# Kernel tuning notes

Hardware: AMD Instinct MI355X
Metric: run time of the kernel (lower is better)

The kernel has to match this reference:

```python
import jax, jax.numpy as jnp
import numpy as np

B, S, H, OUT, STEPS = 64, 1024, 512, 256, 32


def setup_inputs() -> dict:
    key = jax.random.key(0)
    ks = jax.random.split(key, 10)
    s = 0.02
    return {
        "encoder_outputs": jax.random.normal(ks[0], (B, S, H), jnp.float32),
        "hidden": jax.random.normal(ks[1], (B, H), jnp.float32),
        # Attention: nn.Linear(2H, 1)
        "attn_w": jax.random.normal(ks[2], (2 * H,), jnp.float32) * s,
        "attn_b": jax.random.normal(ks[3], (1,), jnp.float32) * s,
        # LSTMCell(OUT + H, H): torch gate order i, f, g, o
        "w_ih": jax.random.normal(ks[4], (4 * H, OUT + H), jnp.float32) * s,
        "w_hh": jax.random.normal(ks[5], (4 * H, H), jnp.float32) * s,
        "b_ih": jax.random.normal(ks[6], (4 * H,), jnp.float32) * s,
        "b_hh": jax.random.normal(ks[7], (4 * H,), jnp.float32) * s,
        # fc: nn.Linear(H, OUT)
        "fc_w": jax.random.normal(ks[8], (OUT, H), jnp.float32) * s,
        "fc_b": jax.random.normal(ks[9], (OUT,), jnp.float32) * s,
    }


def reference(encoder_outputs, hidden, attn_w, attn_b, w_ih, w_hh, b_ih, b_hh, fc_w, fc_b):
    # Split attention weight: Linear(concat(enc, hid)) == enc@wa_e + hid@wa_d + b
    wa_e, wa_d = attn_w[:H], attn_w[H:]
    # encoder contribution to attention energy is step-invariant: [B, S]
    enc_energy = jnp.einsum("bsh,h->bs", encoder_outputs, wa_e) + attn_b[0]
    bias = b_ih + b_hh  # [4H]

    def step(carry, _):
        h, c, dec_in = carry
        # Bahdanau-style energy and context
        energy = enc_energy + (h @ wa_d)[:, None]          # [B, S]
        weights = jax.nn.softmax(energy, axis=1)
        context = jnp.einsum("bs,bsh->bh", weights, encoder_outputs)
        # LSTMCell (torch gate order i, f, g, o)
        x = jnp.concatenate([dec_in, context], axis=1)     # [B, OUT+H]
        gates = x @ w_ih.T + h @ w_hh.T + bias             # [B, 4H]
        i, f, g, o = jnp.split(gates, 4, axis=1)
        c_new = jax.nn.sigmoid(f) * c + jax.nn.sigmoid(i) * jnp.tanh(g)
        h_new = jax.nn.sigmoid(o) * jnp.tanh(c_new)
        dec_new = h_new @ fc_w.T + fc_b                    # [B, OUT]
        return (h_new, c_new, dec_new), dec_new

    dec0 = jnp.zeros((encoder_outputs.shape[0], fc_w.shape[0]), encoder_outputs.dtype)
    c0 = jnp.zeros_like(hidden)
    _, outs = jax.lax.scan(step, (hidden, c0, dec0), None, length=STEPS)
    return jnp.transpose(outs, (1, 0, 2))  # [B, STEPS, OUT]
```

## Files before the change

kernel.cpp:

```cpp
#include <hip/hip_runtime.h>
#include <math.h>

#define B 64
#define S 1024
#define H 512
#define OUT 256
#define STEPS 32
#define NG 2048
#define X 768

typedef __attribute__((ext_vector_type(8))) short short8;
typedef __attribute__((ext_vector_type(4))) short s16x4;
typedef __attribute__((ext_vector_type(4))) float f32x4;
typedef __attribute__((ext_vector_type(4))) unsigned u32x4;

__device__ __forceinline__ float sigf(float x) { return 1.0f / (1.0f + __expf(-x)); }
__device__ __forceinline__ float tanhf_fast(float x) {
  return 2.0f / (1.0f + __expf(-2.0f * x)) - 1.0f;
}

__device__ __forceinline__ short f2bf(float x) {
  union { float f; unsigned u; } a; a.f = x;
  unsigned r = a.u + 0x7fffu + ((a.u >> 16) & 1u);
  return (short)(r >> 16);
}
__device__ __forceinline__ float bf2f(short s) {
  union { unsigned u; float f; } a; a.u = ((unsigned)(unsigned short)s) << 16;
  return a.f;
}

__device__ __forceinline__ unsigned load_u32_cg(const unsigned* p) {
  unsigned r;
  asm volatile("global_load_dword %0, %1, off sc0 sc1\n\ts_waitcnt vmcnt(0)"
               : "=v"(r) : "v"(p) : "memory");
  return r;
}

__global__ __launch_bounds__(256) void k_pre(
    const float* __restrict__ enc, const float* __restrict__ attn_w,
    float* __restrict__ part_ctx, float* __restrict__ part_ml,
    const float* __restrict__ w_ih, const float* __restrict__ w_hh,
    const float* __restrict__ fc_w, short* __restrict__ whi,
    short* __restrict__ wlo) {
  __shared__ float smem[8320];
  const int cid = blockIdx.x;
  const int tid = threadIdx.x;
  if (cid < 512) {
    float* sm_acc = smem;
    float* sm_l = smem + 2048;
    const int b = cid >> 3, chunk = cid & 7;
    const int wave = tid >> 6, lane = tid & 63;
    const float4 wa0 = *(const float4*)(attn_w + lane * 8);
    const float4 wa1 = *(const float4*)(attn_w + lane * 8 + 4);
    const float* eb = enc + (long)b * S * H + (long)(chunk * 128 + wave) * H + lane * 8;
    float l = 0.0f;
    float acc[8];
#pragma unroll
    for (int r = 0; r < 8; ++r) acc[r] = 0.0f;
#pragma unroll 2
    for (int i = 0; i < 32; ++i) {
      const float* row = eb + (long)i * 4 * H;
      const float4 v0 = *(const float4*)row;
      const float4 v1 = *(const float4*)(row + 4);
      float e = v0.x * wa0.x + v0.y * wa0.y + v0.z * wa0.z + v0.w * wa0.w +
                v1.x * wa1.x + v1.y * wa1.y + v1.z * wa1.z + v1.w * wa1.w;
#pragma unroll
      for (int msk = 1; msk < 64; msk <<= 1) e += __shfl_xor(e, msk, 64);
      const float p = __expf(e);
      l += p;
      acc[0] = fmaf(p, v0.x, acc[0]); acc[1] = fmaf(p, v0.y, acc[1]);
      acc[2] = fmaf(p, v0.z, acc[2]); acc[3] = fmaf(p, v0.w, acc[3]);
      acc[4] = fmaf(p, v1.x, acc[4]); acc[5] = fmaf(p, v1.y, acc[5]);
      acc[6] = fmaf(p, v1.z, acc[6]); acc[7] = fmaf(p, v1.w, acc[7]);
    }
#pragma unroll
    for (int r = 0; r < 8; ++r) sm_acc[wave * 512 + lane * 8 + r] = acc[r];
    if (lane == 0) sm_l[wave] = l;
    __syncthreads();
    const int h0 = tid * 2;
    float s0 = 0.f, s1 = 0.f;
#pragma unroll
    for (int w = 0; w < 4; ++w) {
      s0 += sm_acc[w * 512 + h0];
      s1 += sm_acc[w * 512 + h0 + 1];
    }
    float* pc = part_ctx + ((long)chunk * B + b) * H;
    pc[h0] = s0; pc[h0 + 1] = s1;
    if (tid == 0)
      part_ml[chunk * B + b] = sm_l[0] + sm_l[1] + sm_l[2] + sm_l[3];
  } else {
    float* ft = smem;
    float* wd = smem + 4128;
    const int n0 = (cid - 512) * 16;
    for (int i = tid; i < 1024; i += 256) {
      const int r = i >> 6, c4 = (i & 63) << 2;
      *(float4*)&wd[r * 260 + c4] = *(const float4*)(w_ih + (long)(n0 + r) * X + c4);
    }
    float acc[2][16];
#pragma unroll
    for (int rg = 0; rg < 2; ++rg)
#pragma unroll
      for (int e = 0; e < 16; ++e) acc[rg][e] = 0.f;
    const int n_l = tid >> 5, kq = tid & 31;
    for (int jt = 0; jt < 32; ++jt) {
      __syncthreads();
      for (int i = tid; i < 1024; i += 256) {
        const int r = i >> 7, c4 = (i & 127) << 2;
        *(float4*)&ft[r * 516 + c4] =
            *(const float4*)(fc_w + (long)(jt * 8 + r) * H + c4);
      }
      __syncthreads();
#pragma unroll 2
      for (int j = 0; j < 8; ++j) {
        float4 f[4];
#pragma unroll
        for (int e4 = 0; e4 < 4; ++e4) f[e4] = *(float4*)&ft[j * 516 + kq * 4 + e4 * 128];
#pragma unroll
        for (int rg = 0; rg < 2; ++rg) {
          const float w = wd[(rg * 8 + n_l) * 260 + jt * 8 + j];
#pragma unroll
          for (int e4 = 0; e4 < 4; ++e4) {
            acc[rg][e4 * 4 + 0] = fmaf(w, f[e4].x, acc[rg][e4 * 4 + 0]);
            acc[rg][e4 * 4 + 1] = fmaf(w, f[e4].y, acc[rg][e4 * 4 + 1]);
            acc[rg][e4 * 4 + 2] = fmaf(w, f[e4].z, acc[rg][e4 * 4 + 2]);
            acc[rg][e4 * 4 + 3] = fmaf(w, f[e4].w, acc[rg][e4 * 4 + 3]);
          }
        }
      }
    }
#pragma unroll
    for (int rg = 0; rg < 2; ++rg) {
      const long rbase = (long)(n0 + rg * 8 + n_l) * H;
#pragma unroll
      for (int e4 = 0; e4 < 4; ++e4) {
        const int k = kq * 4 + e4 * 128;
        const float4 hh = *(const float4*)(w_hh + rbase + k);
        float v[4] = {acc[rg][e4 * 4] + hh.x, acc[rg][e4 * 4 + 1] + hh.y,
                      acc[rg][e4 * 4 + 2] + hh.z, acc[rg][e4 * 4 + 3] + hh.w};
        s16x4 hi4, lo4;
#pragma unroll
        for (int e = 0; e < 4; ++e) {
          const short hb = f2bf(v[e]);
          hi4[e] = hb;
          lo4[e] = f2bf(v[e] - bf2f(hb));
        }
        *(s16x4*)(whi + rbase + k) = hi4;
        *(s16x4*)(wlo + rbase + k) = lo4;
      }
    }
  }
}

__global__ __launch_bounds__(256) void k_gbase(
    const float* __restrict__ w_ih, const float* __restrict__ w_hh,
    const float* __restrict__ b_ih, const float* __restrict__ b_hh,
    const float* __restrict__ fc_b, const float* __restrict__ part_ctx,
    const float* __restrict__ part_ml, const float* __restrict__ hidden,
    float* __restrict__ gates0, float* __restrict__ gbase2) {
  __shared__ float wt[128][33];
  __shared__ float rb[16][524];
  __shared__ float sfc[256];
  __shared__ float sfL[16];
  const int n0 = blockIdx.x * 32, b0 = blockIdx.y * 16;
  const int tid = threadIdx.x;
  const int n_l = tid & 31, bh = tid >> 5;
  const int n = n0 + n_l;

  if (tid < 16) {
    float L = 0.f;
#pragma unroll
    for (int c = 0; c < 8; ++c) L += part_ml[c * B + b0 + tid];
    sfL[tid] = 1.0f / L;
  }
  sfc[tid] = fc_b[tid];
  __syncthreads();

  for (int i = tid; i < 16 * 128; i += 256) {
    const int r = i >> 7, c4 = (i & 127) << 2;
    float4 s = {0.f, 0.f, 0.f, 0.f};
#pragma unroll
    for (int c8 = 0; c8 < 8; ++c8) {
      const float4 p = *(const float4*)(part_ctx + ((long)c8 * B + b0 + r) * H + c4);
      s.x += p.x; s.y += p.y; s.z += p.z; s.w += p.w;
    }
    const float inv = sfL[r];
    s.x *= inv; s.y *= inv; s.z *= inv; s.w *= inv;
    *(float4*)&rb[r][c4] = s;
  }

  float a1a = 0.f, a1b = 0.f;
  for (int kc = 0; kc < 4; ++kc) {
    __syncthreads();
    for (int i = tid; i < 4096; i += 256) {
      const int r = i >> 7, c = i & 127;
      wt[c][r] = w_ih[(long)(n0 + r) * X + OUT + kc * 128 + c];
    }
    __syncthreads();
#pragma unroll 8
    for (int k = 0; k < 128; ++k) {
      const float wv = wt[k][n_l];
      a1a = fmaf(wv, rb[bh][kc * 128 + k], a1a);
      a1b = fmaf(wv, rb[bh + 8][kc * 128 + k], a1b);
    }
  }

  float db = 0.f;
  for (int kc = 0; kc < 2; ++kc) {
    __syncthreads();
    for (int i = tid; i < 4096; i += 256) {
      const int r = i >> 7, c = i & 127;
      wt[c][r] = w_ih[(long)(n0 + r) * X + kc * 128 + c];
    }
    __syncthreads();
#pragma unroll 8
    for (int k = 0; k < 128; ++k) db = fmaf(wt[k][n_l], sfc[kc * 128 + k], db);
  }

  __syncthreads();
  for (int i = tid; i < 16 * 128; i += 256) {
    const int r = i >> 7, c = (i & 127) << 2;
    *(float4*)&rb[r][c] = *(const float4*)(hidden + (long)(b0 + r) * H + c);
  }
  float a2a = 0.f, a2b = 0.f;
  for (int kc = 0; kc < 4; ++kc) {
    __syncthreads();
    for (int i = tid; i < 4096; i += 256) {
      const int r = i >> 7, c = i & 127;
      wt[c][r] = w_hh[(long)(n0 + r) * H + kc * 128 + c];
    }
    __syncthreads();
#pragma unroll 8
    for (int k = 0; k < 128; ++k) {
      const float wv = wt[k][n_l];
      a2a = fmaf(wv, rb[bh][kc * 128 + k], a2a);
      a2b = fmaf(wv, rb[bh + 8][kc * 128 + k], a2b);
    }
  }

  const float bias = b_ih[n] + b_hh[n];
  gates0[(long)(b0 + bh) * NG + n]     = a1a + bias + a2a;
  gates0[(long)(b0 + bh + 8) * NG + n] = a1b + bias + a2b;
  gbase2[(long)(b0 + bh) * NG + n]     = a1a + bias + db;
  gbase2[(long)(b0 + bh + 8) * NG + n] = a1b + bias + db;
}

#define HSTR 520
__global__ __launch_bounds__(256, 1) void k_recur3(
    const short* __restrict__ whi, const short* __restrict__ wlo,
    const float* __restrict__ gb2, const float* __restrict__ gates0,
    unsigned* __restrict__ hsbf, unsigned int* __restrict__ bar) {
  __shared__ short sh_hi[16 * HSTR];
  __shared__ short sh_lo[16 * HSTR];
  __shared__ float sG[4][8][20];
  __shared__ float sgb[8][64];
  __shared__ float scell[8][16];
  __shared__ int s_fast;

  const int blk = blockIdx.x;
  const int bg = blk & 7;
  const int slice = blk >> 3;
  const int b8 = bg << 3;
  const int hc0 = slice << 4;
  const int tid = threadIdx.x;
  const int w = tid >> 6, l = tid & 63;
  const int ln = l & 15, lk = l >> 4;

  if (tid == 0) {
    unsigned xcc;
    asm volatile("s_getreg_b32 %0, hwreg(20, 0, 32)" : "=s"(xcc));
    __hip_atomic_fetch_or(&bar[7936 + bg], 1u << (xcc & 0xFu),
                          __ATOMIC_RELEASE, __HIP_MEMORY_SCOPE_AGENT);
    unsigned* gbar = &bar[7944 + bg];
    __hip_atomic_fetch_add(gbar, 1u, __ATOMIC_RELEASE, __HIP_MEMORY_SCOPE_AGENT);
    while (load_u32_cg(gbar) < 32u) __builtin_amdgcn_s_sleep(1);
    const unsigned mask = __hip_atomic_load(&bar[7936 + bg], __ATOMIC_ACQUIRE,
                                            __HIP_MEMORY_SCOPE_AGENT);
    s_fast = (__popc(mask) == 1) ? 1 : 0;
  }
  __syncthreads();
  const bool fast = (s_fast != 0);

  for (int i = tid; i < 16 * HSTR; i += 256) { sh_hi[i] = 0; sh_lo[i] = 0; }

  for (int idx = tid; idx < 512; idx += 256) {
    const int b = idx >> 6, gr = idx & 63, g = gr >> 4, j = gr & 15;
    sgb[b][gr] = gb2[(long)(b8 + b) * NG + (g << 9) + hc0 + j];
  }

  short8 wh[16], wl[16];
  {
    const long wb = (long)((w << 9) + hc0 + ln) * H + (lk << 3);
#pragma unroll
    for (int kk = 0; kk < 16; ++kk) {
      wh[kk] = *(const short8*)(whi + wb + kk * 32);
      wl[kk] = *(const short8*)(wlo + wb + kk * 32);
    }
  }
  __syncthreads();

  if (tid < 128) {
    const int b = tid >> 4, j = tid & 15;
    const float* g0 = gates0 + (long)(b8 + b) * NG + hc0 + j;
    const float gi = g0[0];
    const float gg = g0[1024];
    const float go = g0[1536];
    const float cn = sigf(gi) * tanhf_fast(gg);
    const float hn = sigf(go) * tanhf_fast(cn);
    scell[b][j] = cn;
    const short hi = f2bf(hn);
    const short lo = f2bf(hn - bf2f(hi));
    hsbf[(long)(b8 + b) * H + hc0 + j] =
        (unsigned)(unsigned short)hi | ((unsigned)(unsigned short)lo << 16);
    asm volatile("s_waitcnt vmcnt(0)" ::: "memory");
  }
  __syncthreads();
  if (tid == 0) {
    unsigned* f0 = bar + bg * 32;
    if (fast)
      __hip_atomic_fetch_add(&f0[slice], 1u, __ATOMIC_RELAXED, __HIP_MEMORY_SCOPE_AGENT);
    else
      __hip_atomic_fetch_add(&f0[slice], 1u, __ATOMIC_RELEASE, __HIP_MEMORY_SCOPE_AGENT);
  }

  for (int t = 1; t < STEPS; ++t) {
    unsigned* flags = bar + (t - 1) * 256 + bg * 32;
    const unsigned* hb = hsbf + (long)(t - 1) * B * H + (long)b8 * H;
    if (fast) {
      const unsigned* fl = flags + (w << 3);
      while (!__all(load_u32_cg(fl + (l & 7)) != 0u)) {}
      const int colu = (w << 7) + ((l & 31) << 2);
      const int r0 = (l >> 5) << 2;
#pragma unroll
      for (int q = 0; q < 4; ++q) {
        const int row = r0 + q;
        const u32x4 v = *(const u32x4*)(hb + (long)row * H + colu);
        s16x4 hi4, lo4;
#pragma unroll
        for (int e = 0; e < 4; ++e) {
          hi4[e] = (short)(v[e] & 0xFFFFu);
          lo4[e] = (short)(v[e] >> 16);
        }
        *(s16x4*)&sh_hi[row * HSTR + colu] = hi4;
        *(s16x4*)&sh_lo[row * HSTR + colu] = lo4;
      }
    } else {
      if (tid < 64) {
        while (!__all(load_u32_cg(flags + (tid & 31)) != 0u)) {}
      }
      if (tid == 0)
        (void)__hip_atomic_load(&flags[0], __ATOMIC_ACQUIRE, __HIP_MEMORY_SCOPE_AGENT);
      __syncthreads();
#pragma unroll
      for (int q = 0; q < 4; ++q) {
        const int d0 = q * 1024 + tid * 4;
        const u32x4 v = *(const u32x4*)(hb + d0);
        const int row = d0 >> 9, col = d0 & 511;
        s16x4 hi4, lo4;
#pragma unroll
        for (int e = 0; e < 4; ++e) {
          hi4[e] = (short)(v[e] & 0xFFFFu);
          lo4[e] = (short)(v[e] >> 16);
        }
        *(s16x4*)&sh_hi[row * HSTR + col] = hi4;
        *(s16x4*)&sh_lo[row * HSTR + col] = lo4;
      }
    }
    __syncthreads();

    f32x4 a0 = {0.f, 0.f, 0.f, 0.f};
    f32x4 a1 = {0.f, 0.f, 0.f, 0.f};
    f32x4 a2 = {0.f, 0.f, 0.f, 0.f};
    asm volatile("s_nop 3" ::);
    const int abase = ln * HSTR + (lk << 3);
#pragma unroll
    for (int kk = 0; kk < 16; ++kk) {
      const short8 ah = *(const short8*)&sh_hi[abase + kk * 32];
      const short8 al = *(const short8*)&sh_lo[abase + kk * 32];
      asm volatile("v_mfma_f32_16x16x32_bf16 %0, %1, %2, %0"
                   : "+v"(a0) : "v"(ah), "a"(wh[kk]));
      asm volatile("v_mfma_f32_16x16x32_bf16 %0, %1, %2, %0"
                   : "+v"(a1) : "v"(al), "a"(wh[kk]));
      asm volatile("v_mfma_f32_16x16x32_bf16 %0, %1, %2, %0"
                   : "+v"(a2) : "v"(ah), "a"(wl[kk]));
    }
    asm volatile("s_nop 7\n\ts_nop 7" ::);
    if (lk < 2) {
#pragma unroll
      for (int r = 0; r < 4; ++r)
        sG[w][(lk << 2) + r][ln] = a0[r] + a1[r] + a2[r];
    }
    __syncthreads();

    if (tid < 128) {
      const int b = tid >> 4, j = tid & 15;
      const float gi = sG[0][b][j] + sgb[b][j];
      const float gf = sG[1][b][j] + sgb[b][16 + j];
      const float gg = sG[2][b][j] + sgb[b][32 + j];
      const float go = sG[3][b][j] + sgb[b][48 + j];
      const float c_old = scell[b][j];
      const float cn = sigf(gf) * c_old + sigf(gi) * tanhf_fast(gg);
      const float hn = sigf(go) * tanhf_fast(cn);
      scell[b][j] = cn;
      const short hi = f2bf(hn);
      const short lo = f2bf(hn - bf2f(hi));
      hsbf[(long)t * B * H + (long)(b8 + b) * H + hc0 + j] =
          (unsigned)(unsigned short)hi | ((unsigned)(unsigned short)lo << 16);
      asm volatile("s_waitcnt vmcnt(0)" ::: "memory");
    }
    __syncthreads();

    if (t < STEPS - 1) {
      if (tid == 0) {
        unsigned* nf = bar + t * 256 + bg * 32;
        if (fast)
          __hip_atomic_fetch_add(&nf[slice], 1u, __ATOMIC_RELAXED,
                                 __HIP_MEMORY_SCOPE_AGENT);
        else
          __hip_atomic_fetch_add(&nf[slice], 1u, __ATOMIC_RELEASE,
                                 __HIP_MEMORY_SCOPE_AGENT);
      }
    }
  }
}

__global__ __launch_bounds__(256) void k_dec2(
    const unsigned* __restrict__ hsbf, const float* __restrict__ fc_w,
    const float* __restrict__ fc_b, float* __restrict__ out) {
  __shared__ float A[32 * 68];
  __shared__ float Bm[64 * 68];
  const int m0 = blockIdx.x * 32;
  const int o0 = blockIdx.y * 64;
  const int tid = threadIdx.x;
  const int tn = tid & 15, tm = tid >> 4;
  float acc[2][4] = {{0.f, 0.f, 0.f, 0.f}, {0.f, 0.f, 0.f, 0.f}};
  for (int k0 = 0; k0 < H; k0 += 64) {
    for (int idx = tid; idx < 512; idx += 256) {
      const int r = idx >> 4, k4 = idx & 15;
      const u32x4 v = *(const u32x4*)&hsbf[(long)(m0 + r) * H + k0 + k4 * 4];
#pragma unroll
      for (int e = 0; e < 4; ++e)
        A[r * 68 + k4 * 4 + e] =
            bf2f((short)(v[e] & 0xFFFFu)) + bf2f((short)(v[e] >> 16));
    }
    for (int idx = tid; idx < 1024; idx += 256) {
      const int r = idx >> 4, k4 = idx & 15;
      *(float4*)&Bm[r * 68 + k4 * 4] =
          *(const float4*)&fc_w[(long)(o0 + r) * H + k0 + k4 * 4];
    }
    __syncthreads();
#pragma unroll
    for (int k4 = 0; k4 < 16; ++k4) {
      const float4 a0 = *(float4*)&A[tm * 68 + k4 * 4];
      const float4 a1 = *(float4*)&A[(tm + 16) * 68 + k4 * 4];
      const float4 b0 = *(float4*)&Bm[tn * 68 + k4 * 4];
      const float4 b1 = *(float4*)&Bm[(tn + 16) * 68 + k4 * 4];
      const float4 b2 = *(float4*)&Bm[(tn + 32) * 68 + k4 * 4];
      const float4 b3 = *(float4*)&Bm[(tn + 48) * 68 + k4 * 4];
      acc[0][0] += a0.x * b0.x + a0.y * b0.y + a0.z * b0.z + a0.w * b0.w;
      acc[0][1] += a0.x * b1.x + a0.y * b1.y + a0.z * b1.z + a0.w * b1.w;
      acc[0][2] += a0.x * b2.x + a0.y * b2.y + a0.z * b2.z + a0.w * b2.w;
      acc[0][3] += a0.x * b3.x + a0.y * b3.y + a0.z * b3.z + a0.w * b3.w;
      acc[1][0] += a1.x * b0.x + a1.y * b0.y + a1.z * b0.z + a1.w * b0.w;
      acc[1][1] += a1.x * b1.x + a1.y * b1.y + a1.z * b1.z + a1.w * b1.w;
      acc[1][2] += a1.x * b2.x + a1.y * b2.y + a1.z * b2.z + a1.w * b2.w;
      acc[1][3] += a1.x * b3.x + a1.y * b3.y + a1.z * b3.z + a1.w * b3.w;
    }
    __syncthreads();
  }
#pragma unroll
  for (int i = 0; i < 2; ++i) {
    const int m = m0 + tm + 16 * i;
    const int t = m >> 6, b = m & 63;
#pragma unroll
    for (int j = 0; j < 4; ++j) {
      const int o = o0 + tn + 16 * j;
      out[((long)b * STEPS + t) * OUT + o] = acc[i][j] + fc_b[o];
    }
  }
}

extern "C" void kernel_launch(void* const* d_in, const int* in_sizes, int n_in,
                              void* d_out, int out_size, void* d_ws, size_t ws_size,
                              hipStream_t stream) {
  const float* enc = (const float*)d_in[0];
  const float* hidden = (const float*)d_in[1];
  const float* attn_w = (const float*)d_in[2];
  const float* w_ih = (const float*)d_in[4];
  const float* w_hh = (const float*)d_in[5];
  const float* b_ih = (const float*)d_in[6];
  const float* b_hh = (const float*)d_in[7];
  const float* fc_w = (const float*)d_in[8];
  const float* fc_b = (const float*)d_in[9];
  float* out = (float*)d_out;

  float* ws = (float*)d_ws;
  float* part_ctx = ws;
  float* part_ml  = part_ctx + 262144;
  short* whi      = (short*)(part_ml + 1024);
  short* wlo      = whi + 1048576;
  float* gates0   = (float*)(wlo + 1048576);
  float* gbase2   = gates0 + 131072;
  unsigned* hsbf  = (unsigned*)(gbase2 + 131072);
  unsigned int* bar = (unsigned int*)(hsbf + 1048576);

  hipMemsetAsync(bar, 0, 7952 * sizeof(unsigned int), stream);
  k_pre<<<640, 256, 0, stream>>>(enc, attn_w, part_ctx, part_ml,
                                 w_ih, w_hh, fc_w, whi, wlo);
  k_gbase<<<dim3(64, 4), 256, 0, stream>>>(w_ih, w_hh, b_ih, b_hh, fc_b,
                                           part_ctx, part_ml, hidden,
                                           gates0, gbase2);

  k_recur3<<<256, 256, 0, stream>>>(whi, wlo, gbase2, gates0, hsbf, bar);

  k_dec2<<<dim3(64, 4), 256, 0, stream>>>(hsbf, fc_w, fc_b, out);
}
```

Baseline: 254.7 us.

## Widen pre-pass parallelism and add separate context reduction kernel

The encoder pass in k_pre now uses 512-thread blocks over 16 sequence chunks, giving 1024 attention blocks instead of 512. The weight-fusion blocks now handle one row group per thread. A new k_ctx_sum kernel reduces the partial contexts and normalizers once per batch row, so k_gbase no longer repeats that reduction in every block. The partial buffers are placed in the hsbf workspace region to save memory. This adds a kernel launch and more partial traffic in exchange for more parallelism in the memory-bound encoder read.

Measured after the change: 250.1 us. Within noise of the previous version (-1.8%).

```diff
diff --git a/kernel.cpp b/kernel.cpp
--- a/kernel.cpp
+++ b/kernel.cpp
@@ -36,30 +36,30 @@
   return r;
 }
 
-__global__ __launch_bounds__(256) void k_pre(
+__global__ __launch_bounds__(512) void k_pre(
     const float* __restrict__ enc, const float* __restrict__ attn_w,
     float* __restrict__ part_ctx, float* __restrict__ part_ml,
     const float* __restrict__ w_ih, const float* __restrict__ w_hh,
     const float* __restrict__ fc_w, short* __restrict__ whi,
     short* __restrict__ wlo) {
-  __shared__ float smem[8320];
+  __shared__ float smem[8288];
   const int cid = blockIdx.x;
   const int tid = threadIdx.x;
-  if (cid < 512) {
+  if (cid < 1024) {
     float* sm_acc = smem;
-    float* sm_l = smem + 2048;
-    const int b = cid >> 3, chunk = cid & 7;
+    float* sm_l = smem + 4096;
+    const int b = cid >> 4, chunk = cid & 15;
     const int wave = tid >> 6, lane = tid & 63;
     const float4 wa0 = *(const float4*)(attn_w + lane * 8);
     const float4 wa1 = *(const float4*)(attn_w + lane * 8 + 4);
-    const float* eb = enc + (long)b * S * H + (long)(chunk * 128 + wave) * H + lane * 8;
+    const float* eb = enc + (long)b * S * H + (long)(chunk * 64 + wave) * H + lane * 8;
     float l = 0.0f;
     float acc[8];
 #pragma unroll
     for (int r = 0; r < 8; ++r) acc[r] = 0.0f;
-#pragma unroll 2
-    for (int i = 0; i < 32; ++i) {
-      const float* row = eb + (long)i * 4 * H;
+#pragma unroll
+    for (int i = 0; i < 8; ++i) {
+      const float* row = eb + (long)i * 8 * H;
       const float4 v0 = *(const float4*)row;
       const float4 v1 = *(const float4*)(row + 4);
       float e = v0.x * wa0.x + v0.y * wa0.y + v0.z * wa0.z + v0.w * wa0.w +
@@ -77,34 +77,31 @@
     for (int r = 0; r < 8; ++r) sm_acc[wave * 512 + lane * 8 + r] = acc[r];
     if (lane == 0) sm_l[wave] = l;
     __syncthreads();
-    const int h0 = tid * 2;
-    float s0 = 0.f, s1 = 0.f;
-#pragma unroll
-    for (int w = 0; w < 4; ++w) {
-      s0 += sm_acc[w * 512 + h0];
-      s1 += sm_acc[w * 512 + h0 + 1];
-    }
-    float* pc = part_ctx + ((long)chunk * B + b) * H;
-    pc[h0] = s0; pc[h0 + 1] = s1;
-    if (tid == 0)
-      part_ml[chunk * B + b] = sm_l[0] + sm_l[1] + sm_l[2] + sm_l[3];
+    float s = 0.f;
+#pragma unroll
+    for (int w = 0; w < 8; ++w) s += sm_acc[w * 512 + tid];
+    part_ctx[((long)chunk * B + b) * H + tid] = s;
+    if (tid == 0) {
+      float L = 0.f;
+#pragma unroll
+      for (int w = 0; w < 8; ++w) L += sm_l[w];
+      part_ml[chunk * B + b] = L;
+    }
   } else {
     float* ft = smem;
     float* wd = smem + 4128;
-    const int n0 = (cid - 512) * 16;
-    for (int i = tid; i < 1024; i += 256) {
+    const int n0 = (cid - 1024) * 16;
+    for (int i = tid; i < 1024; i += 512) {
       const int r = i >> 6, c4 = (i & 63) << 2;
       *(float4*)&wd[r * 260 + c4] = *(const float4*)(w_ih + (long)(n0 + r) * X + c4);
     }
-    float acc[2][16];
-#pragma unroll
-    for (int rg = 0; rg < 2; ++rg)
-#pragma unroll
-      for (int e = 0; e < 16; ++e) acc[rg][e] = 0.f;
+    float acc[16];
+#pragma unroll
+    for (int e = 0; e < 16; ++e) acc[e] = 0.f;
     const int n_l = tid >> 5, kq = tid & 31;
     for (int jt = 0; jt < 32; ++jt) {
       __syncthreads();
-      for (int i = tid; i < 1024; i += 256) {
+      for (int i = tid; i < 1024; i += 512) {
         const int r = i >> 7, c4 = (i & 127) << 2;
         *(float4*)&ft[r * 516 + c4] =
             *(const float4*)(fc_w + (long)(jt * 8 + r) * H + c4);
@@ -112,80 +109,74 @@
       __syncthreads();
 #pragma unroll 2
       for (int j = 0; j < 8; ++j) {
-        float4 f[4];
-#pragma unroll
-        for (int e4 = 0; e4 < 4; ++e4) f[e4] = *(float4*)&ft[j * 516 + kq * 4 + e4 * 128];
-#pragma unroll
-        for (int rg = 0; rg < 2; ++rg) {
-          const float w = wd[(rg * 8 + n_l) * 260 + jt * 8 + j];
-#pragma unroll
-          for (int e4 = 0; e4 < 4; ++e4) {
-            acc[rg][e4 * 4 + 0] = fmaf(w, f[e4].x, acc[rg][e4 * 4 + 0]);
-            acc[rg][e4 * 4 + 1] = fmaf(w, f[e4].y, acc[rg][e4 * 4 + 1]);
-            acc[rg][e4 * 4 + 2] = fmaf(w, f[e4].z, acc[rg][e4 * 4 + 2]);
-            acc[rg][e4 * 4 + 3] = fmaf(w, f[e4].w, acc[rg][e4 * 4 + 3]);
-          }
+        const float w = wd[n_l * 260 + jt * 8 + j];
+#pragma unroll
+        for (int e4 = 0; e4 < 4; ++e4) {
+          const float4 f = *(float4*)&ft[j * 516 + kq * 4 + e4 * 128];
+          acc[e4 * 4 + 0] = fmaf(w, f.x, acc[e4 * 4 + 0]);
+          acc[e4 * 4 + 1] = fmaf(w, f.y, acc[e4 * 4 + 1]);
+          acc[e4 * 4 + 2] = fmaf(w, f.z, acc[e4 * 4 + 2]);
+          acc[e4 * 4 + 3] = fmaf(w, f.w, acc[e4 * 4 + 3]);
         }
       }
     }
-#pragma unroll
-    for (int rg = 0; rg < 2; ++rg) {
-      const long rbase = (long)(n0 + rg * 8 + n_l) * H;
-#pragma unroll
-      for (int e4 = 0; e4 < 4; ++e4) {
-        const int k = kq * 4 + e4 * 128;
-        const float4 hh = *(const float4*)(w_hh + rbase + k);
-        float v[4] = {acc[rg][e4 * 4] + hh.x, acc[rg][e4 * 4 + 1] + hh.y,
-                      acc[rg][e4 * 4 + 2] + hh.z, acc[rg][e4 * 4 + 3] + hh.w};
-        s16x4 hi4, lo4;
-#pragma unroll
-        for (int e = 0; e < 4; ++e) {
-          const short hb = f2bf(v[e]);
-          hi4[e] = hb;
-          lo4[e] = f2bf(v[e] - bf2f(hb));
-        }
-        *(s16x4*)(whi + rbase + k) = hi4;
-        *(s16x4*)(wlo + rbase + k) = lo4;
-      }
-    }
-  }
+    const long rbase = (long)(n0 + n_l) * H;
+#pragma unroll
+    for (int e4 = 0; e4 < 4; ++e4) {
+      const int k = kq * 4 + e4 * 128;
+      const float4 hh = *(const float4*)(w_hh + rbase + k);
+      float v[4] = {acc[e4 * 4] + hh.x, acc[e4 * 4 + 1] + hh.y,
+                    acc[e4 * 4 + 2] + hh.z, acc[e4 * 4 + 3] + hh.w};
+      s16x4 hi4, lo4;
+#pragma unroll
+      for (int e = 0; e < 4; ++e) {
+        const short hb = f2bf(v[e]);
+        hi4[e] = hb;
+        lo4[e] = f2bf(v[e] - bf2f(hb));
+      }
+      *(s16x4*)(whi + rbase + k) = hi4;
+      *(s16x4*)(wlo + rbase + k) = lo4;
+    }
+  }
+}
+
+__global__ __launch_bounds__(256) void k_ctx_sum(
+    const float* __restrict__ part_ctx, const float* __restrict__ part_ml,
+    float* __restrict__ ctx) {
+  const int b = blockIdx.x;
+  float L = 0.f;
+#pragma unroll
+  for (int c = 0; c < 16; ++c) L += part_ml[c * B + b];
+  const float inv = 1.0f / L;
+  const int h0 = threadIdx.x * 2;
+  float s0 = 0.f, s1 = 0.f;
+#pragma unroll
+  for (int c = 0; c < 16; ++c) {
+    const float* pc = part_ctx + ((long)c * B + b) * H;
+    s0 += pc[h0]; s1 += pc[h0 + 1];
+  }
+  ctx[(long)b * H + h0] = s0 * inv;
+  ctx[(long)b * H + h0 + 1] = s1 * inv;
 }
 
 __global__ __launch_bounds__(256) void k_gbase(
     const float* __restrict__ w_ih, const float* __restrict__ w_hh,
     const float* __restrict__ b_ih, const float* __restrict__ b_hh,
-    const float* __restrict__ fc_b, const float* __restrict__ part_ctx,
-    const float* __restrict__ part_ml, const float* __restrict__ hidden,
-    float* __restrict__ gates0, float* __restrict__ gbase2) {
+    const float* __restrict__ fc_b, const float* __restrict__ ctx,
+    const float* __restrict__ hidden, float* __restrict__ gates0,
+    float* __restrict__ gbase2) {
   __shared__ float wt[128][33];
   __shared__ float rb[16][524];
   __shared__ float sfc[256];
-  __shared__ float sfL[16];
   const int n0 = blockIdx.x * 32, b0 = blockIdx.y * 16;
   const int tid = threadIdx.x;
   const int n_l = tid & 31, bh = tid >> 5;
   const int n = n0 + n_l;
 
-  if (tid < 16) {
-    float L = 0.f;
-#pragma unroll
-    for (int c = 0; c < 8; ++c) L += part_ml[c * B + b0 + tid];
-    sfL[tid] = 1.0f / L;
-  }
   sfc[tid] = fc_b[tid];
-  __syncthreads();
-
   for (int i = tid; i < 16 * 128; i += 256) {
     const int r = i >> 7, c4 = (i & 127) << 2;
-    float4 s = {0.f, 0.f, 0.f, 0.f};
-#pragma unroll
-    for (int c8 = 0; c8 < 8; ++c8) {
-      const float4 p = *(const float4*)(part_ctx + ((long)c8 * B + b0 + r) * H + c4);
-      s.x += p.x; s.y += p.y; s.z += p.z; s.w += p.w;
-    }
-    const float inv = sfL[r];
-    s.x *= inv; s.y *= inv; s.z *= inv; s.w *= inv;
-    *(float4*)&rb[r][c4] = s;
+    *(float4*)&rb[r][c4] = *(const float4*)(ctx + (long)(b0 + r) * H + c4);
   }
 
   float a1a = 0.f, a1b = 0.f;
@@ -494,21 +485,22 @@
   float* out = (float*)d_out;
 
   float* ws = (float*)d_ws;
-  float* part_ctx = ws;
-  float* part_ml  = part_ctx + 262144;
-  short* whi      = (short*)(part_ml + 1024);
+  short* whi      = (short*)ws;
   short* wlo      = whi + 1048576;
   float* gates0   = (float*)(wlo + 1048576);
   float* gbase2   = gates0 + 131072;
   unsigned* hsbf  = (unsigned*)(gbase2 + 131072);
-  unsigned int* bar = (unsigned int*)(hsbf + 1048576);
+  float* part_ctx = (float*)hsbf;
+  float* part_ml  = (float*)(hsbf + 1048576);
+  float* ctx      = part_ml + 1024;
+  unsigned int* bar = (unsigned int*)(ctx + 32768);
 
   hipMemsetAsync(bar, 0, 7952 * sizeof(unsigned int), stream);
-  k_pre<<<640, 256, 0, stream>>>(enc, attn_w, part_ctx, part_ml,
-                                 w_ih, w_hh, fc_w, whi, wlo);
-  k_gbase<<<dim3(64, 4), 256, 0, stream>>>(w_ih, w_hh, b_ih, b_hh, fc_b,
-                                           part_ctx, part_ml, hidden,
-                                           gates0, gbase2);
+  k_pre<<<1152, 512, 0, stream>>>(enc, attn_w, part_ctx, part_ml,
+                                  w_ih, w_hh, fc_w, whi, wlo);
+  k_ctx_sum<<<64, 256, 0, stream>>>(part_ctx, part_ml, ctx);
+  k_gbase<<<dim3(64, 4), 256, 0, stream>>>(w_ih, w_hh, b_ih, b_hh, fc_b, ctx,
+                                           hidden, gates0, gbase2);
 
   k_recur3<<<256, 256, 0, stream>>>(whi, wlo, gbase2, gates0, hsbf, bar);
 
```
